# Optimization experiments

Hardware: AMD Instinct MI355X
Metric: run time of the kernel (lower is better)

The kernel has to match this reference:

```python
import jax, jax.numpy as jnp
import numpy as np

TEMP = 0.07
POS_WINDOW = 2
EPS = 1e-8
NEG = -1e9  # finite large-negative for masking (safe under vjp)


def _l2norm(x):
    # matches F.normalize(dim=-1) with eps=1e-12
    n = jnp.sqrt(jnp.sum(x * x, axis=-1, keepdims=True))
    return x / jnp.maximum(n, 1e-12)


def setup_inputs() -> dict:
    key = jax.random.key(0)
    k1, k2, k3, k4, k5 = jax.random.split(key, 5)
    B, T, D = 32, 1024, 256
    eeg_enc = jax.random.normal(k1, (B, T, D), dtype=jnp.float32)
    eye_enc = jax.random.normal(k2, (B, T, D), dtype=jnp.float32)
    mask = jax.random.randint(k3, (B, T), 0, 2, dtype=jnp.int32)
    W_eeg = jax.random.normal(k4, (D, D), dtype=jnp.float32) / np.sqrt(D)
    W_eye = jax.random.normal(k5, (D, D), dtype=jnp.float32) / np.sqrt(D)
    return {"eeg_enc": eeg_enc, "eye_enc": eye_enc, "mask": mask,
            "W_eeg": W_eeg, "W_eye": W_eye}


def reference(eeg_enc, eye_enc, mask, W_eeg, W_eye):
    B, T, D = eeg_enc.shape
    valid = mask > 0  # (B,T)
    # nn.Linear(bias=False): x @ W.T, then L2-normalize
    e = _l2norm(jnp.einsum('btd,ed->bte', eeg_enc, W_eeg))
    v = _l2norm(jnp.einsum('btd,ed->bte', eye_enc, W_eye))
    sims = jnp.einsum('bid,bjd->bij', e, v) / TEMP  # (B,T,T)
    # rank of each valid step within the compressed (gathered) ordering
    rank = jnp.cumsum(valid.astype(jnp.int32), axis=-1) - 1  # (B,T)
    band = jnp.abs(rank[:, :, None] - rank[:, None, :]) <= POS_WINDOW
    pair = valid[:, :, None] & valid[:, None, :]  # both steps valid
    pos = pair & band
    # per-row max over positive (banded) entries
    pos_scores = jnp.max(jnp.where(pos, sims, NEG), axis=-1)  # (B,T)
    # logsumexp over valid columns (the gathered sims row)
    lse = jax.nn.logsumexp(jnp.where(valid[:, None, :], sims, NEG), axis=-1)
    row_loss = -(pos_scores - lse)  # (B,T)
    Tv = jnp.sum(valid, axis=-1)  # (B,)
    per_b = jnp.sum(jnp.where(valid, row_loss, 0.0), axis=-1) / jnp.maximum(Tv, 1)
    per_b = jnp.where(Tv >= 2, per_b, 0.0)  # skip samples with <2 valid steps
    return jnp.sum(per_b) / (B + EPS)
```

## Files before the change

kernel.cpp:

```cpp
#include <hip/hip_runtime.h>
#include <hip/hip_bf16.h>

typedef __attribute__((ext_vector_type(8))) short bf16x8;
typedef __attribute__((ext_vector_type(4))) float f32x4;

#define INVT (1.0f/0.07f)

static __device__ __forceinline__ short f2bf(float f){
    unsigned int u = __float_as_uint(f);
    unsigned int r = (u + 0x7fffu + ((u >> 16) & 1u)) >> 16;
    return (short)r;
}
static __device__ __forceinline__ float bf2f(short s){
    return __uint_as_float(((unsigned int)(unsigned short)s) << 16);
}

static __device__ __forceinline__ void gld16(const void* g, void* l){
    __builtin_amdgcn_global_load_lds(
        (const __attribute__((address_space(1))) unsigned int*)g,
        (__attribute__((address_space(3))) unsigned int*)l, 16, 0, 0);
}

__global__ __launch_bounds__(256) void prep_kernel(const float* __restrict__ Weeg,
                                                   const float* __restrict__ Weye,
                                                   const int* __restrict__ mask,
                                                   short* __restrict__ Wout,
                                                   int* __restrict__ rank,
                                                   int* __restrict__ idx,
                                                   int* __restrict__ Tv,
                                                   float* __restrict__ cb,
                                                   float* __restrict__ bsum){
    __shared__ int ssum[256];
    int tid = threadIdx.x;
    if (blockIdx.x < 512){
        int i = blockIdx.x * 256 + tid;
        float v = (i < 65536) ? Weeg[i] : Weye[i - 65536];
        Wout[i] = f2bf(v);
        return;
    }
    int b = blockIdx.x - 512;
    if (tid == 0) bsum[b] = 0.f;
    int local[4]; int s = 0;
    #pragma unroll
    for (int q = 0; q < 4; ++q){
        int t = tid*4 + q;
        local[q] = (mask[b*1024 + t] > 0) ? 1 : 0;
        s += local[q];
    }
    ssum[tid] = s;
    __syncthreads();
    for (int off = 1; off < 256; off <<= 1){
        int add = (tid >= off) ? ssum[tid - off] : 0;
        __syncthreads();
        ssum[tid] += add;
        __syncthreads();
    }
    int run = ssum[tid] - s;
    #pragma unroll
    for (int q = 0; q < 4; ++q){
        int t = tid*4 + q;
        int g = b*1024 + t;
        run += local[q];
        rank[g] = run - 1;
        cb[g]   = local[q] ? 0.0f : -1e9f;
        if (local[q]) idx[b*1024 + run - 1] = t;
    }
    if (tid == 255) Tv[b] = ssum[255];
}

__global__ __launch_bounds__(256, 2) void proj_kernel(const float* __restrict__ Aeeg,
                                                      const float* __restrict__ Aeye,
                                                      const short* __restrict__ Wbf,
                                                      short* __restrict__ Eout,
                                                      short* __restrict__ Vout){
    __shared__ short sW[2][64 * 256];
    int sel = blockIdx.y;
    const float* A   = sel ? Aeye : Aeeg;
    const short* W   = Wbf + sel * 65536;
    short*       Out = sel ? Vout : Eout;

    int tid = threadIdx.x;
    int w = tid >> 6, lane = tid & 63;
    int l15 = lane & 15, lq = lane >> 4;
    int kb  = lq * 8;
    int row0 = blockIdx.x * 64;

    int ro   = lane >> 5;
    int cs   = lane & 31;
    int s7   = l15 & 7;

    #pragma unroll
    for (int p = 0; p < 8; ++p){
        int rr = (p*2 + ro) & 7;
        gld16(W + (size_t)(w*16 + p*2 + ro)*256 + (cs ^ rr)*8,
              &sW[0][(w*16 + p*2) * 256]);
    }
    #pragma unroll
    for (int p = 0; p < 8; ++p){
        int rr = (p*2 + ro) & 7;
        gld16(W + (size_t)(64 + w*16 + p*2 + ro)*256 + (cs ^ rr)*8,
              &sW[1][(w*16 + p*2) * 256]);
    }

    bf16x8 xf[8];
    {
        const float* ap = A + (size_t)(row0 + w*16 + l15) * 256 + kb;
        #pragma unroll
        for (int g = 0; g < 8; ++g){
            float4 x0 = *(const float4*)(ap + g*32);
            float4 x1 = *(const float4*)(ap + g*32 + 4);
            bf16x8 t;
            t[0]=f2bf(x0.x); t[1]=f2bf(x0.y); t[2]=f2bf(x0.z); t[3]=f2bf(x0.w);
            t[4]=f2bf(x1.x); t[5]=f2bf(x1.y); t[6]=f2bf(x1.z); t[7]=f2bf(x1.w);
            xf[g] = t;
        }
    }

    f32x4 acc[16];
    #pragma unroll
    for (int q = 0; q < 16; ++q) acc[q] = (f32x4){0.f,0.f,0.f,0.f};

    __syncthreads();

    #pragma unroll
    for (int nt = 0; nt < 4; ++nt){
        f32x4 c = acc[nt];
        int rbase = (nt*16 + l15) * 256;
        #pragma unroll
        for (int g = 0; g < 8; ++g){
            bf16x8 wf = *(const bf16x8*)&sW[0][rbase + (((g*4 + lq) ^ s7) << 3)];
            c = __builtin_amdgcn_mfma_f32_16x16x32_bf16(wf, xf[g], c, 0, 0, 0);
        }
        acc[nt] = c;
    }

    __syncthreads();

    #pragma unroll
    for (int p = 0; p < 8; ++p){
        int rr = (p*2 + ro) & 7;
        gld16(W + (size_t)(128 + w*16 + p*2 + ro)*256 + (cs ^ rr)*8,
              &sW[0][(w*16 + p*2) * 256]);
    }
    #pragma unroll
    for (int nt = 0; nt < 4; ++nt){
        f32x4 c = acc[4 + nt];
        int rbase = (nt*16 + l15) * 256;
        #pragma unroll
        for (int g = 0; g < 8; ++g){
            bf16x8 wf = *(const bf16x8*)&sW[1][rbase + (((g*4 + lq) ^ s7) << 3)];
            c = __builtin_amdgcn_mfma_f32_16x16x32_bf16(wf, xf[g], c, 0, 0, 0);
        }
        acc[4 + nt] = c;
    }

    __syncthreads();

    #pragma unroll
    for (int p = 0; p < 8; ++p){
        int rr = (p*2 + ro) & 7;
        gld16(W + (size_t)(192 + w*16 + p*2 + ro)*256 + (cs ^ rr)*8,
              &sW[1][(w*16 + p*2) * 256]);
    }
    #pragma unroll
    for (int nt = 0; nt < 4; ++nt){
        f32x4 c = acc[8 + nt];
        int rbase = (nt*16 + l15) * 256;
        #pragma unroll
        for (int g = 0; g < 8; ++g){
            bf16x8 wf = *(const bf16x8*)&sW[0][rbase + (((g*4 + lq) ^ s7) << 3)];
            c = __builtin_amdgcn_mfma_f32_16x16x32_bf16(wf, xf[g], c, 0, 0, 0);
        }
        acc[8 + nt] = c;
    }

    __syncthreads();

    #pragma unroll
    for (int nt = 0; nt < 4; ++nt){
        f32x4 c = acc[12 + nt];
        int rbase = (nt*16 + l15) * 256;
        #pragma unroll
        for (int g = 0; g < 8; ++g){
            bf16x8 wf = *(const bf16x8*)&sW[1][rbase + (((g*4 + lq) ^ s7) << 3)];
            c = __builtin_amdgcn_mfma_f32_16x16x32_bf16(wf, xf[g], c, 0, 0, 0);
        }
        acc[12 + nt] = c;
    }

    float ss = 0.f;
    #pragma unroll
    for (int q = 0; q < 16; ++q){
        #pragma unroll
        for (int r = 0; r < 4; ++r){ float x = acc[q][r]; ss += x*x; }
    }
    ss += __shfl_xor(ss, 16);
    ss += __shfl_xor(ss, 32);
    float scale = 1.0f / fmaxf(sqrtf(ss), 1e-12f);

    short* twrow = &sW[0][(w*16 + l15) * 256];
    #pragma unroll
    for (int q = 0; q < 16; ++q){
        short4 pk;
        pk.x = f2bf(acc[q][0] * scale);
        pk.y = f2bf(acc[q][1] * scale);
        pk.z = f2bf(acc[q][2] * scale);
        pk.w = f2bf(acc[q][3] * scale);
        int c    = (q >> 2) * 64 + (q & 3) * 16 + lq*4;
        int blk  = (c >> 3) ^ s7;
        *(short4*)(twrow + blk*8 + (c & 7)) = pk;
    }
    short* op = Out + (size_t)(row0 + w*16) * 256;
    #pragma unroll
    for (int p = 0; p < 8; ++p){
        int rloc = p*2 + (lane >> 5);
        int gblk = lane & 31;
        const short* tr = &sW[0][(w*16 + rloc) * 256 + ((gblk ^ (rloc & 7)) * 8)];
        *(int4*)(op + rloc*256 + gblk*8) = *(const int4*)tr;
    }
}

__global__ __launch_bounds__(256, 2) void loss_kernel(const short* __restrict__ E,
                                                      const short* __restrict__ V,
                                                      const float* __restrict__ cb,
                                                      float* __restrict__ psum){
    __shared__ short sV[2][64 * 256];
    __shared__ float sRed[4][32];

    int n  = blockIdx.x;
    int m  = n >> 3;
    int b  = ((m >> 5) << 3) | (n & 7);
    int lm = m & 31;
    int i0 = (lm >> 2) * 128;
    int js = lm & 3;
    int j0 = js * 256;

    int tid = threadIdx.x;
    int w = tid >> 6, lane = tid & 63;
    int l15 = lane & 15, lq = lane >> 4;
    int kb = lq * 8;
    int s7 = l15 & 7;
    int ro = lane >> 5;
    int cs = lane & 31;

    const short* Vrow = V + ((size_t)b*1024 + j0 + w*16 + ro) * 256;

    #pragma unroll
    for (int p = 0; p < 8; ++p){
        int rr = (p*2 + ro) & 7;
        gld16(Vrow + (size_t)(p*2)*256 + (size_t)((cs ^ rr) * 8),
              &sV[0][(w*16 + p*2) * 256]);
    }

    bf16x8 af[2][8];
    {
        const short* ep = E + ((size_t)b*1024 + i0 + w*32 + l15) * 256 + kb;
        #pragma unroll
        for (int g = 0; g < 8; ++g){
            af[0][g] = *(const bf16x8*)(ep + g*32);
            af[1][g] = *(const bf16x8*)(ep + 16*256 + g*32);
        }
    }

    float cbv0[8];
    #pragma unroll
    for (int ct = 0; ct < 8; ++ct)
        cbv0[ct] = cb[b*1024 + j0 + ct*16 + l15];

    f32x4 acc[2][8];
    #pragma unroll
    for (int s = 0; s < 2; ++s)
        #pragma unroll
        for (int ct = 0; ct < 8; ++ct) acc[s][ct] = (f32x4){0.f,0.f,0.f,0.f};
    float ls[2][4] = {{0.f,0.f,0.f,0.f},{0.f,0.f,0.f,0.f}};

    __syncthreads();

    #pragma unroll
    for (int p = 0; p < 8; ++p){
        int rr = (p*2 + ro) & 7;
        gld16(Vrow + (size_t)(64 + p*2)*256 + (size_t)((cs ^ rr) * 8),
              &sV[1][(w*16 + p*2) * 256]);
    }
    #pragma unroll
    for (int jt = 0; jt < 4; ++jt){
        bf16x8 bf[8];
        #pragma unroll
        for (int g = 0; g < 8; ++g)
            bf[g] = *(const bf16x8*)&sV[0][(jt*16 + l15)*256 + (((g*4 + lq) ^ s7) << 3)];
        #pragma unroll
        for (int g = 0; g < 8; ++g){
            acc[0][jt] = __builtin_amdgcn_mfma_f32_16x16x32_bf16(af[0][g], bf[g], acc[0][jt], 0, 0, 0);
            acc[1][jt] = __builtin_amdgcn_mfma_f32_16x16x32_bf16(af[1][g], bf[g], acc[1][jt], 0, 0, 0);
        }
    }

    __syncthreads();

    #pragma unroll
    for (int p = 0; p < 8; ++p){
        int rr = (p*2 + ro) & 7;
        gld16(Vrow + (size_t)(128 + p*2)*256 + (size_t)((cs ^ rr) * 8),
              &sV[0][(w*16 + p*2) * 256]);
    }
    #pragma unroll
    for (int jt = 0; jt < 4; ++jt){
        bf16x8 bf[8];
        #pragma unroll
        for (int g = 0; g < 8; ++g)
            bf[g] = *(const bf16x8*)&sV[1][(jt*16 + l15)*256 + (((g*4 + lq) ^ s7) << 3)];
        #pragma unroll
        for (int g = 0; g < 8; ++g){
            acc[0][4+jt] = __builtin_amdgcn_mfma_f32_16x16x32_bf16(af[0][g], bf[g], acc[0][4+jt], 0, 0, 0);
            acc[1][4+jt] = __builtin_amdgcn_mfma_f32_16x16x32_bf16(af[1][g], bf[g], acc[1][4+jt], 0, 0, 0);
        }
    }
    #pragma unroll
    for (int s = 0; s < 2; ++s){
        #pragma unroll
        for (int r = 0; r < 4; ++r){
            float a0 = 0.f;
            #pragma unroll
            for (int ct = 0; ct < 8; ++ct)
                a0 += __expf(fmaf(acc[s][ct][r], INVT, cbv0[ct]));
            ls[s][r] += a0;
        }
    }
    #pragma unroll
    for (int s = 0; s < 2; ++s)
        #pragma unroll
        for (int ct = 0; ct < 8; ++ct) acc[s][ct] = (f32x4){0.f,0.f,0.f,0.f};

    float cbv1[8];
    #pragma unroll
    for (int ct = 0; ct < 8; ++ct)
        cbv1[ct] = cb[b*1024 + j0 + 128 + ct*16 + l15];

    __syncthreads();

    #pragma unroll
    for (int p = 0; p < 8; ++p){
        int rr = (p*2 + ro) & 7;
        gld16(Vrow + (size_t)(192 + p*2)*256 + (size_t)((cs ^ rr) * 8),
              &sV[1][(w*16 + p*2) * 256]);
    }
    #pragma unroll
    for (int jt = 0; jt < 4; ++jt){
        bf16x8 bf[8];
        #pragma unroll
        for (int g = 0; g < 8; ++g)
            bf[g] = *(const bf16x8*)&sV[0][(jt*16 + l15)*256 + (((g*4 + lq) ^ s7) << 3)];
        #pragma unroll
        for (int g = 0; g < 8; ++g){
            acc[0][jt] = __builtin_amdgcn_mfma_f32_16x16x32_bf16(af[0][g], bf[g], acc[0][jt], 0, 0, 0);
            acc[1][jt] = __builtin_amdgcn_mfma_f32_16x16x32_bf16(af[1][g], bf[g], acc[1][jt], 0, 0, 0);
        }
    }

    __syncthreads();

    #pragma unroll
    for (int jt = 0; jt < 4; ++jt){
        bf16x8 bf[8];
        #pragma unroll
        for (int g = 0; g < 8; ++g)
            bf[g] = *(const bf16x8*)&sV[1][(jt*16 + l15)*256 + (((g*4 + lq) ^ s7) << 3)];
        #pragma unroll
        for (int g = 0; g < 8; ++g){
            acc[0][4+jt] = __builtin_amdgcn_mfma_f32_16x16x32_bf16(af[0][g], bf[g], acc[0][4+jt], 0, 0, 0);
            acc[1][4+jt] = __builtin_amdgcn_mfma_f32_16x16x32_bf16(af[1][g], bf[g], acc[1][4+jt], 0, 0, 0);
        }
    }
    #pragma unroll
    for (int s = 0; s < 2; ++s){
        #pragma unroll
        for (int r = 0; r < 4; ++r){
            float a1 = 0.f;
            #pragma unroll
            for (int ct = 0; ct < 8; ++ct)
                a1 += __expf(fmaf(acc[s][ct][r], INVT, cbv1[ct]));
            ls[s][r] += a1;
        }
    }

    #pragma unroll
    for (int s = 0; s < 2; ++s){
        #pragma unroll
        for (int r = 0; r < 4; ++r){
            float v = ls[s][r];
            #pragma unroll
            for (int mm = 1; mm < 16; mm <<= 1)
                v += __shfl_xor(v, mm);
            ls[s][r] = v;
        }
    }
    if (l15 == 0){
        #pragma unroll
        for (int s = 0; s < 2; ++s)
            #pragma unroll
            for (int r = 0; r < 4; ++r)
                sRed[w][s*16 + lq*4 + r] = ls[s][r];
    }
    float* pp = psum + (((size_t)(b*4 + js)) << 10);
    if (lane < 32) pp[i0 + w*32 + lane] = sRed[w][lane];
}

__global__ __launch_bounds__(256) void pos_kernel(const short* __restrict__ E,
                                                  const short* __restrict__ V,
                                                  const int* __restrict__ mask,
                                                  const int* __restrict__ rank,
                                                  const int* __restrict__ idx,
                                                  const int* __restrict__ Tv,
                                                  float* __restrict__ pmax){
    int tid = threadIdx.x;
    int gl  = tid & 15;
    int rf  = (blockIdx.x * 256 + tid) >> 4;
    int b   = rf >> 10;
    if (mask[rf] <= 0) return;

    int ri = rank[rf];
    int tv = Tv[b];
    int lo = ri - 2; if (lo < 0) lo = 0;
    int hi = ri + 2; if (hi > tv - 1) hi = tv - 1;

    const short* epp = E + (size_t)rf * 256 + gl * 16;
    float ev[16];
    {
        bf16x8 e0 = *(const bf16x8*)epp;
        bf16x8 e1 = *(const bf16x8*)(epp + 8);
        #pragma unroll
        for (int k = 0; k < 8; ++k){ ev[k] = bf2f(e0[k]); ev[8+k] = bf2f(e1[k]); }
    }
    float pm = -1e30f;
    for (int r = lo; r <= hi; ++r){
        int j = idx[b*1024 + r];
        const short* vpp = V + ((size_t)(b*1024) + j) * 256 + gl * 16;
        bf16x8 v0 = *(const bf16x8*)vpp;
        bf16x8 v1 = *(const bf16x8*)(vpp + 8);
        float s = 0.f;
        #pragma unroll
        for (int k = 0; k < 8; ++k){
            s = fmaf(ev[k],   bf2f(v0[k]), s);
            s = fmaf(ev[8+k], bf2f(v1[k]), s);
        }
        s += __shfl_xor(s, 1);
        s += __shfl_xor(s, 2);
        s += __shfl_xor(s, 4);
        s += __shfl_xor(s, 8);
        pm = fmaxf(pm, s);
    }
    if (gl == 0) pmax[rf] = pm * INVT;
}

__global__ __launch_bounds__(256) void reduce_kernel(const float* __restrict__ psum,
                                                     const float* __restrict__ pmax,
                                                     const int* __restrict__ mask,
                                                     float* __restrict__ bsum){
    int b  = blockIdx.x >> 2;
    int i  = (blockIdx.x & 3) * 256 + threadIdx.x;
    int g  = b*1024 + i;
    float a = 0.f;
    if (mask[g] > 0){
        const float* pp = psum + ((size_t)b << 12);
        float ps = pp[i] + pp[i + 1024] + pp[i + 2048] + pp[i + 3072];
        a = logf(ps) - pmax[g];
    }
    #pragma unroll
    for (int m = 1; m < 64; m <<= 1) a += __shfl_xor(a, m);
    if ((threadIdx.x & 63) == 0 && a != 0.f) atomicAdd(&bsum[b], a);
}

__global__ void final_kernel(const float* __restrict__ bsum,
                             const int* __restrict__ Tv,
                             float* __restrict__ out){
    int tid = threadIdx.x;
    float v = 0.f;
    if (tid < 32){
        int tv = Tv[tid];
        if (tv >= 2) v = bsum[tid] / (float)tv;
    }
    #pragma unroll
    for (int m = 1; m < 64; m <<= 1) v += __shfl_xor(v, m);
    if (tid == 0) out[0] = v / 32.0f;
}

extern "C" void kernel_launch(void* const* d_in, const int* in_sizes, int n_in,
                              void* d_out, int out_size, void* d_ws, size_t ws_size,
                              hipStream_t stream) {
    const float* eeg  = (const float*)d_in[0];
    const float* eye  = (const float*)d_in[1];
    const int*   mask = (const int*)d_in[2];
    const float* Weeg = (const float*)d_in[3];
    const float* Weye = (const float*)d_in[4];
    float* out = (float*)d_out;

    char* ws = (char*)d_ws;
    short* e_bf  = (short*)(ws);
    short* v_bf  = (short*)(ws + 16777216);
    short* wbf   = (short*)(ws + 33554432);
    int*   rank  = (int*)  (ws + 33816576);
    int*   idx   = (int*)  (ws + 33947648);
    float* cb    = (float*)(ws + 34078720);
    float* psum  = (float*)(ws + 34209792);
    float* pmax  = (float*)(ws + 34734080);
    int*   Tv    = (int*)  (ws + 34865152);
    float* bsum  = (float*)(ws + 34865280);

    prep_kernel<<<544, 256, 0, stream>>>(Weeg, Weye, mask, wbf, rank, idx, Tv, cb, bsum);
    proj_kernel<<<dim3(512, 2), 256, 0, stream>>>(eeg, eye, wbf, e_bf, v_bf);
    loss_kernel<<<1024, 256, 0, stream>>>(e_bf, v_bf, cb, psum);
    pos_kernel<<<2048, 256, 0, stream>>>(e_bf, v_bf, mask, rank, idx, Tv, pmax);
    reduce_kernel<<<128, 256, 0, stream>>>(psum, pmax, mask, bsum);
    final_kernel<<<1, 64, 0, stream>>>(bsum, Tv, out);
}
```

Baseline: 159.1 us.

## Rewrite loss kernel as single-wave blocks streaming V from global via registers

The loss kernel now runs one 64-lane wave per block. Each wave holds 64 rows of E in registers and streams 512 V columns straight from global memory with register double-buffering, replacing the shared-memory staging and the block barriers. The column split drops from four partials to two, and the reduce kernel is updated to match. This removes LDS traffic and synchronisation, but relies on L2/cache hits for the repeated V reads, uses more registers per wave, and gives fewer waves for latency hiding.

```diff
diff --git a/kernel.cpp b/kernel.cpp
--- a/kernel.cpp
+++ b/kernel.cpp
@@ -220,171 +220,102 @@
     }
 }
 
-__global__ __launch_bounds__(256, 2) void loss_kernel(const short* __restrict__ E,
-                                                      const short* __restrict__ V,
-                                                      const float* __restrict__ cb,
-                                                      float* __restrict__ psum){
-    __shared__ short sV[2][64 * 256];
-    __shared__ float sRed[4][32];
-
+__global__ __launch_bounds__(64) void loss_kernel(const short* __restrict__ E,
+                                                  const short* __restrict__ V,
+                                                  const float* __restrict__ cb,
+                                                  float* __restrict__ psum){
     int n  = blockIdx.x;
-    int m  = n >> 3;
-    int b  = ((m >> 5) << 3) | (n & 7);
-    int lm = m & 31;
-    int i0 = (lm >> 2) * 128;
-    int js = lm & 3;
-    int j0 = js * 256;
-
-    int tid = threadIdx.x;
-    int w = tid >> 6, lane = tid & 63;
+    int b  = (((n >> 3) & 3) << 3) | (n & 7);
+    int r2 = n >> 5;
+    int it = r2 & 15;
+    int jh = r2 >> 4;
+
+    int lane = threadIdx.x;
     int l15 = lane & 15, lq = lane >> 4;
-    int kb = lq * 8;
-    int s7 = l15 & 7;
-    int ro = lane >> 5;
-    int cs = lane & 31;
-
-    const short* Vrow = V + ((size_t)b*1024 + j0 + w*16 + ro) * 256;
-
-    #pragma unroll
-    for (int p = 0; p < 8; ++p){
-        int rr = (p*2 + ro) & 7;
-        gld16(Vrow + (size_t)(p*2)*256 + (size_t)((cs ^ rr) * 8),
-              &sV[0][(w*16 + p*2) * 256]);
-    }
-
-    bf16x8 af[2][8];
+
+    bf16x8 af[4][8];
     {
-        const short* ep = E + ((size_t)b*1024 + i0 + w*32 + l15) * 256 + kb;
-        #pragma unroll
-        for (int g = 0; g < 8; ++g){
-            af[0][g] = *(const bf16x8*)(ep + g*32);
-            af[1][g] = *(const bf16x8*)(ep + 16*256 + g*32);
-        }
-    }
-
-    float cbv0[8];
-    #pragma unroll
-    for (int ct = 0; ct < 8; ++ct)
-        cbv0[ct] = cb[b*1024 + j0 + ct*16 + l15];
-
-    f32x4 acc[2][8];
-    #pragma unroll
-    for (int s = 0; s < 2; ++s)
-        #pragma unroll
-        for (int ct = 0; ct < 8; ++ct) acc[s][ct] = (f32x4){0.f,0.f,0.f,0.f};
-    float ls[2][4] = {{0.f,0.f,0.f,0.f},{0.f,0.f,0.f,0.f}};
-
-    __syncthreads();
-
-    #pragma unroll
-    for (int p = 0; p < 8; ++p){
-        int rr = (p*2 + ro) & 7;
-        gld16(Vrow + (size_t)(64 + p*2)*256 + (size_t)((cs ^ rr) * 8),
-              &sV[1][(w*16 + p*2) * 256]);
-    }
-    #pragma unroll
-    for (int jt = 0; jt < 4; ++jt){
-        bf16x8 bf[8];
-        #pragma unroll
-        for (int g = 0; g < 8; ++g)
-            bf[g] = *(const bf16x8*)&sV[0][(jt*16 + l15)*256 + (((g*4 + lq) ^ s7) << 3)];
-        #pragma unroll
-        for (int g = 0; g < 8; ++g){
-            acc[0][jt] = __builtin_amdgcn_mfma_f32_16x16x32_bf16(af[0][g], bf[g], acc[0][jt], 0, 0, 0);
-            acc[1][jt] = __builtin_amdgcn_mfma_f32_16x16x32_bf16(af[1][g], bf[g], acc[1][jt], 0, 0, 0);
-        }
-    }
-
-    __syncthreads();
-
-    #pragma unroll
-    for (int p = 0; p < 8; ++p){
-        int rr = (p*2 + ro) & 7;
-        gld16(Vrow + (size_t)(128 + p*2)*256 + (size_t)((cs ^ rr) * 8),
-              &sV[0][(w*16 + p*2) * 256]);
-    }
-    #pragma unroll
-    for (int jt = 0; jt < 4; ++jt){
-        bf16x8 bf[8];
-        #pragma unroll
-        for (int g = 0; g < 8; ++g)
-            bf[g] = *(const bf16x8*)&sV[1][(jt*16 + l15)*256 + (((g*4 + lq) ^ s7) << 3)];
-        #pragma unroll
-        for (int g = 0; g < 8; ++g){
-            acc[0][4+jt] = __builtin_amdgcn_mfma_f32_16x16x32_bf16(af[0][g], bf[g], acc[0][4+jt], 0, 0, 0);
-            acc[1][4+jt] = __builtin_amdgcn_mfma_f32_16x16x32_bf16(af[1][g], bf[g], acc[1][4+jt], 0, 0, 0);
-        }
-    }
-    #pragma unroll
-    for (int s = 0; s < 2; ++s){
-        #pragma unroll
-        for (int r = 0; r < 4; ++r){
-            float a0 = 0.f;
-            #pragma unroll
-            for (int ct = 0; ct < 8; ++ct)
-                a0 += __expf(fmaf(acc[s][ct][r], INVT, cbv0[ct]));
-            ls[s][r] += a0;
-        }
-    }
-    #pragma unroll
-    for (int s = 0; s < 2; ++s)
-        #pragma unroll
-        for (int ct = 0; ct < 8; ++ct) acc[s][ct] = (f32x4){0.f,0.f,0.f,0.f};
-
-    float cbv1[8];
-    #pragma unroll
-    for (int ct = 0; ct < 8; ++ct)
-        cbv1[ct] = cb[b*1024 + j0 + 128 + ct*16 + l15];
-
-    __syncthreads();
-
-    #pragma unroll
-    for (int p = 0; p < 8; ++p){
-        int rr = (p*2 + ro) & 7;
-        gld16(Vrow + (size_t)(192 + p*2)*256 + (size_t)((cs ^ rr) * 8),
-              &sV[1][(w*16 + p*2) * 256]);
-    }
-    #pragma unroll
-    for (int jt = 0; jt < 4; ++jt){
-        bf16x8 bf[8];
-        #pragma unroll
-        for (int g = 0; g < 8; ++g)
-            bf[g] = *(const bf16x8*)&sV[0][(jt*16 + l15)*256 + (((g*4 + lq) ^ s7) << 3)];
-        #pragma unroll
-        for (int g = 0; g < 8; ++g){
-            acc[0][jt] = __builtin_amdgcn_mfma_f32_16x16x32_bf16(af[0][g], bf[g], acc[0][jt], 0, 0, 0);
-            acc[1][jt] = __builtin_amdgcn_mfma_f32_16x16x32_bf16(af[1][g], bf[g], acc[1][jt], 0, 0, 0);
-        }
-    }
-
-    __syncthreads();
-
-    #pragma unroll
-    for (int jt = 0; jt < 4; ++jt){
-        bf16x8 bf[8];
-        #pragma unroll
-        for (int g = 0; g < 8; ++g)
-            bf[g] = *(const bf16x8*)&sV[1][(jt*16 + l15)*256 + (((g*4 + lq) ^ s7) << 3)];
-        #pragma unroll
-        for (int g = 0; g < 8; ++g){
-            acc[0][4+jt] = __builtin_amdgcn_mfma_f32_16x16x32_bf16(af[0][g], bf[g], acc[0][4+jt], 0, 0, 0);
-            acc[1][4+jt] = __builtin_amdgcn_mfma_f32_16x16x32_bf16(af[1][g], bf[g], acc[1][4+jt], 0, 0, 0);
-        }
-    }
-    #pragma unroll
-    for (int s = 0; s < 2; ++s){
-        #pragma unroll
-        for (int r = 0; r < 4; ++r){
-            float a1 = 0.f;
-            #pragma unroll
-            for (int ct = 0; ct < 8; ++ct)
-                a1 += __expf(fmaf(acc[s][ct][r], INVT, cbv1[ct]));
-            ls[s][r] += a1;
-        }
-    }
-
-    #pragma unroll
-    for (int s = 0; s < 2; ++s){
+        const short* ep = E + ((size_t)b*1024 + it*64 + l15) * 256 + lq*8;
+        #pragma unroll
+        for (int s = 0; s < 4; ++s)
+            #pragma unroll
+            for (int g = 0; g < 8; ++g)
+                af[s][g] = *(const bf16x8*)(ep + s*16*256 + g*32);
+    }
+
+    const short* vp  = V  + ((size_t)b*1024 + jh*512 + l15) * 256 + lq*8;
+    const float* cbp = cb + b*1024 + jh*512 + l15;
+
+    float ls[4][4];
+    #pragma unroll
+    for (int s = 0; s < 4; ++s)
+        #pragma unroll
+        for (int r = 0; r < 4; ++r) ls[s][r] = 0.f;
+
+    bf16x8 ba[8], bb[8];
+    #pragma unroll
+    for (int g = 0; g < 8; ++g) ba[g] = *(const bf16x8*)(vp + g*32);
+    float ca = cbp[0];
+    float cbv;
+
+    #pragma unroll 1
+    for (int t = 0; t < 16; ++t){
+        {
+            const short* v1 = vp + (size_t)(2*t + 1) * 16 * 256;
+            #pragma unroll
+            for (int g = 0; g < 8; ++g) bb[g] = *(const bf16x8*)(v1 + g*32);
+            cbv = cbp[(2*t + 1) * 16];
+        }
+        {
+            f32x4 a0 = (f32x4){0.f,0.f,0.f,0.f};
+            f32x4 a1 = (f32x4){0.f,0.f,0.f,0.f};
+            f32x4 a2 = (f32x4){0.f,0.f,0.f,0.f};
+            f32x4 a3 = (f32x4){0.f,0.f,0.f,0.f};
+            #pragma unroll
+            for (int g = 0; g < 8; ++g){
+                a0 = __builtin_amdgcn_mfma_f32_16x16x32_bf16(af[0][g], ba[g], a0, 0, 0, 0);
+                a1 = __builtin_amdgcn_mfma_f32_16x16x32_bf16(af[1][g], ba[g], a1, 0, 0, 0);
+                a2 = __builtin_amdgcn_mfma_f32_16x16x32_bf16(af[2][g], ba[g], a2, 0, 0, 0);
+                a3 = __builtin_amdgcn_mfma_f32_16x16x32_bf16(af[3][g], ba[g], a3, 0, 0, 0);
+            }
+            #pragma unroll
+            for (int r = 0; r < 4; ++r){
+                ls[0][r] += __expf(fmaf(a0[r], INVT, ca));
+                ls[1][r] += __expf(fmaf(a1[r], INVT, ca));
+                ls[2][r] += __expf(fmaf(a2[r], INVT, ca));
+                ls[3][r] += __expf(fmaf(a3[r], INVT, ca));
+            }
+        }
+        if (t < 15){
+            const short* v2 = vp + (size_t)(2*t + 2) * 16 * 256;
+            #pragma unroll
+            for (int g = 0; g < 8; ++g) ba[g] = *(const bf16x8*)(v2 + g*32);
+            ca = cbp[(2*t + 2) * 16];
+        }
+        {
+            f32x4 a0 = (f32x4){0.f,0.f,0.f,0.f};
+            f32x4 a1 = (f32x4){0.f,0.f,0.f,0.f};
+            f32x4 a2 = (f32x4){0.f,0.f,0.f,0.f};
+            f32x4 a3 = (f32x4){0.f,0.f,0.f,0.f};
+            #pragma unroll
+            for (int g = 0; g < 8; ++g){
+                a0 = __builtin_amdgcn_mfma_f32_16x16x32_bf16(af[0][g], bb[g], a0, 0, 0, 0);
+                a1 = __builtin_amdgcn_mfma_f32_16x16x32_bf16(af[1][g], bb[g], a1, 0, 0, 0);
+                a2 = __builtin_amdgcn_mfma_f32_16x16x32_bf16(af[2][g], bb[g], a2, 0, 0, 0);
+                a3 = __builtin_amdgcn_mfma_f32_16x16x32_bf16(af[3][g], bb[g], a3, 0, 0, 0);
+            }
+            #pragma unroll
+            for (int r = 0; r < 4; ++r){
+                ls[0][r] += __expf(fmaf(a0[r], INVT, cbv));
+                ls[1][r] += __expf(fmaf(a1[r], INVT, cbv));
+                ls[2][r] += __expf(fmaf(a2[r], INVT, cbv));
+                ls[3][r] += __expf(fmaf(a3[r], INVT, cbv));
+            }
+        }
+    }
+
+    #pragma unroll
+    for (int s = 0; s < 4; ++s)
         #pragma unroll
         for (int r = 0; r < 4; ++r){
             float v = ls[s][r];
@@ -393,16 +324,15 @@
                 v += __shfl_xor(v, mm);
             ls[s][r] = v;
         }
-    }
+
     if (l15 == 0){
-        #pragma unroll
-        for (int s = 0; s < 2; ++s)
+        float* pp = psum + (size_t)jh*32768 + (size_t)b*1024 + it*64;
+        #pragma unroll
+        for (int s = 0; s < 4; ++s)
             #pragma unroll
             for (int r = 0; r < 4; ++r)
-                sRed[w][s*16 + lq*4 + r] = ls[s][r];
-    }
-    float* pp = psum + (((size_t)(b*4 + js)) << 10);
-    if (lane < 32) pp[i0 + w*32 + lane] = sRed[w][lane];
+                pp[s*16 + lq*4 + r] = ls[s][r];
+    }
 }
 
 __global__ __launch_bounds__(256) void pos_kernel(const short* __restrict__ E,
@@ -461,8 +391,7 @@
     int g  = b*1024 + i;
     float a = 0.f;
     if (mask[g] > 0){
-        const float* pp = psum + ((size_t)b << 12);
-        float ps = pp[i] + pp[i + 1024] + pp[i + 2048] + pp[i + 3072];
+        float ps = psum[g] + psum[g + 32768];
         a = logf(ps) - pmax[g];
     }
     #pragma unroll
@@ -508,7 +437,7 @@
 
     prep_kernel<<<544, 256, 0, stream>>>(Weeg, Weye, mask, wbf, rank, idx, Tv, cb, bsum);
     proj_kernel<<<dim3(512, 2), 256, 0, stream>>>(eeg, eye, wbf, e_bf, v_bf);
-    loss_kernel<<<1024, 256, 0, stream>>>(e_bf, v_bf, cb, psum);
+    loss_kernel<<<1024, 64, 0, stream>>>(e_bf, v_bf, cb, psum);
     pos_kernel<<<2048, 256, 0, stream>>>(e_bf, v_bf, mask, rank, idx, Tv, pmax);
     reduce_kernel<<<128, 256, 0, stream>>>(psum, pmax, mask, bsum);
     final_kernel<<<1, 64, 0, stream>>>(bsum, Tv, out);
```

Result: slower. 169.7 us (+6.7%).
